# Kernel optimization log

Hardware: AMD Instinct MI355X
Metric: run time of the kernel (lower is better)

## Reference

```python
import jax, jax.numpy as jnp
import numpy as np

K = 3
STRIDE = 1
PAD = 1


def _conv(x, w, b):
    # NCHW conv, OIHW weight, stride/pad fixed
    y = jax.lax.conv_general_dilated(
        x, w, (STRIDE, STRIDE), [(PAD, PAD), (PAD, PAD)],
        dimension_numbers=("NCHW", "OIHW", "NCHW"))
    if b is not None:
        y = y + b[None, :, None, None]
    return y


def _deform_conv2d(x, offset, mask, weight):
    """torchvision.ops.deform_conv2d (modulated, groups=1, dilation=1, no bias)."""
    B, C, H, W = x.shape
    O = weight.shape[0]
    KK = K * K
    Ho, Wo = offset.shape[2], offset.shape[3]
    off = offset.reshape(B, KK, 2, Ho, Wo)
    off_y, off_x = off[:, :, 0], off[:, :, 1]
    ky = (jnp.arange(KK) // K).astype(x.dtype)  # kernel row offset
    kx = (jnp.arange(KK) % K).astype(x.dtype)   # kernel col offset
    base_y = (jnp.arange(Ho) * STRIDE - PAD).astype(x.dtype)
    base_x = (jnp.arange(Wo) * STRIDE - PAD).astype(x.dtype)
    # sampling positions [B, KK, Ho, Wo]
    py = base_y[None, None, :, None] + ky[None, :, None, None] + off_y
    px = base_x[None, None, None, :] + kx[None, :, None, None] + off_x

    y0 = jnp.floor(py)
    x0 = jnp.floor(px)
    wy = py - y0  # fractional parts
    wx = px - x0

    x_flat = x.reshape(B, C, H * W)

    def gather(yy, xx):
        valid = (yy >= 0) & (yy < H) & (xx >= 0) & (xx < W)
        yc = jnp.clip(yy, 0, H - 1).astype(jnp.int32)
        xc = jnp.clip(xx, 0, W - 1).astype(jnp.int32)
        idx = (yc * W + xc).reshape(B, -1)  # [B, KK*Ho*Wo]
        v = jax.vmap(lambda a, i: a[:, i])(x_flat, idx)  # [B, C, KK*Ho*Wo]
        v = v.reshape(B, C, KK, Ho, Wo)
        return v * valid.astype(x.dtype).reshape(B, 1, KK, Ho, Wo)

    samp = (gather(y0, x0) * ((1 - wy) * (1 - wx))[:, None]
            + gather(y0, x0 + 1) * ((1 - wy) * wx)[:, None]
            + gather(y0 + 1, x0) * (wy * (1 - wx))[:, None]
            + gather(y0 + 1, x0 + 1) * (wy * wx)[:, None])
    samp = samp * mask[:, None]  # modulation [B, C, KK, Ho, Wo]
    return jnp.einsum('bckhw,ock->bohw', samp, weight.reshape(O, C, KK))


def setup_inputs() -> dict:
    key = jax.random.key(0)
    ks = jax.random.split(key, 6)
    B, Cin, H, W, Cout = 4, 128, 128, 128, 256
    KK = K * K
    x = jax.random.normal(ks[0], (B, Cin, H, W), dtype=jnp.float32)
    # offset conv: trained weights are small (init at 0) -> scale down
    offset_w = 0.01 * jax.random.normal(ks[1], (2 * KK, Cin, K, K), dtype=jnp.float32)
    offset_b = 0.1 * jax.random.normal(ks[2], (2 * KK,), dtype=jnp.float32)
    mod_w = 0.1 * jax.random.normal(ks[3], (KK, Cin, K, K), dtype=jnp.float32)
    mod_b = 0.1 * jax.random.normal(ks[4], (KK,), dtype=jnp.float32)
    fan_in = Cin * KK
    weight = jax.random.normal(ks[5], (Cout, Cin, K, K), dtype=jnp.float32) / np.sqrt(fan_in)
    return {"x": x, "offset_w": offset_w, "offset_b": offset_b,
            "mod_w": mod_w, "mod_b": mod_b, "weight": weight}


def reference(x, offset_w, offset_b, mod_w, mod_b, weight):
    offset = _conv(x, offset_w, offset_b)
    modulator = 2.0 * jax.nn.sigmoid(_conv(x, mod_w, mod_b))
    return _deform_conv2d(x, offset, modulator, weight)
```

## Files before the change

### kernel.cpp

```cpp
#include <hip/hip_runtime.h>
#include <hip/hip_bf16.h>
#include <math.h>

#define CIN 128
#define HH 128
#define WW 128
#define HWX (HH*WW)
#define COUT 256
#define NB 4

typedef __attribute__((ext_vector_type(8))) short short8;
typedef __attribute__((ext_vector_type(4))) float f32x4;
typedef __attribute__((ext_vector_type(8))) unsigned short ushort8;

__device__ __forceinline__ unsigned short f2bf(float f) {
    union { float f; unsigned int u; } c; c.f = f;
    unsigned int u = c.u + 0x7FFF + ((c.u >> 16) & 1);
    return (unsigned short)(u >> 16);
}
__device__ __forceinline__ float bf2f(unsigned short u) {
    union { unsigned int u; float f; } c; c.u = ((unsigned int)u) << 16;
    return c.f;
}

__global__ __launch_bounds__(256) void wimg_kernel(
    const float* __restrict__ wgt, unsigned short* __restrict__ wAi)
{
    int i = blockIdx.x * 256 + threadIdx.x;
    int j  = i & 7;
    int l  = (i >> 3) & 63;
    int mt = (i >> 9) & 15;
    int cc = (i >> 13) & 3;
    int kk = i >> 15;
    int o = mt * 16 + (l & 15);
    int c = cc * 32 + (l >> 4) * 8 + j;
    wAi[i] = f2bf(wgt[(o * CIN + c) * 9 + kk]);
}

__global__ __launch_bounds__(256) void wcimg_kernel(
    const float* __restrict__ offw, const float* __restrict__ modw,
    unsigned short* __restrict__ wCi)
{
    int i = blockIdx.x * 256 + threadIdx.x;
    if (i >= 36864) return;
    int j   = i & 7;
    int l   = (i >> 3) & 63;
    int mt  = (i >> 9) & 1;
    int q36 = i >> 10;
    int o = mt * 16 + (l & 15);
    int c = ((q36 & 3) << 5) + ((l >> 4) << 3) + j;
    int t = q36 >> 2;
    float v = 0.f;
    if (o < 18)      v = offw[(o * CIN + c) * 9 + t];
    else if (o < 27) v = modw[((o - 18) * CIN + c) * 9 + t];
    wCi[i] = f2bf(v);
}

__global__ __launch_bounds__(256) void xt_kernel(
    const float* __restrict__ x, float* __restrict__ xT)
{
    __shared__ float ls[32][132];
    const int tid = threadIdx.x;
    const int bz = blockIdx.x;
    const int cg = bz & 3;
    const int y  = (bz >> 2) & 127;
    const int b  = bz >> 9;
    {
        int c  = tid >> 3;
        int x0 = (tid & 7) << 4;
        const float* src = x + (((size_t)(b * CIN + (cg << 5) + c)) << 14) + (y << 7) + x0;
#pragma unroll
        for (int k = 0; k < 4; ++k)
            *(f32x4*)&ls[c][x0 + 4 * k] = *(const f32x4*)(src + 4 * k);
    }
    __syncthreads();
    {
        int xc = tid >> 1;
        int h  = tid & 1;
        float v[16];
#pragma unroll
        for (int j = 0; j < 16; ++j) v[j] = ls[h * 16 + j][xc];
        float* dst = xT + ((((size_t)((b << 7) + y) << 7) + xc) << 7) + (cg << 5) + (h << 4);
#pragma unroll
        for (int k = 0; k < 4; ++k) {
            f32x4 t = { v[4 * k], v[4 * k + 1], v[4 * k + 2], v[4 * k + 3] };
            *(f32x4*)(dst + 4 * k) = t;
        }
    }
}

__global__ __launch_bounds__(256) void convtab_kernel(
    const float* __restrict__ xT, const unsigned short* __restrict__ wCi,
    const float* __restrict__ offb, const float* __restrict__ modb,
    unsigned int* __restrict__ pk_out, float4* __restrict__ w4_out)
{
    __shared__ float outs[4][32][33];
    const int tid = threadIdx.x;
    const int wave = tid >> 6;
    const int l = tid & 63;
    const int bid = blockIdx.x;
    const int b = bid >> 7;
    const int y = bid & 127;
    const int x0 = wave << 5;
    const float* xb = xT + ((size_t)b << 21);

    f32x4 acc[2][2];
#pragma unroll
    for (int i = 0; i < 2; ++i)
#pragma unroll
        for (int j = 0; j < 2; ++j) acc[i][j] = (f32x4){0.f, 0.f, 0.f, 0.f};

    const int lp = l & 15;
    const int q8 = (l >> 4) << 3;

#pragma unroll 1
    for (int q36 = 0; q36 < 36; ++q36) {
        const int t  = q36 >> 2;
        const int c0 = (q36 & 3) << 5;
        const int ty = t / 3, tx = t - 3 * ty;
        const int yp = y + ty - 1;
        if (yp < 0 || yp >= HH) continue;

        const unsigned short* ap = wCi + (q36 << 10) + (l << 3);
        short8 af0 = *(const short8*)(ap);
        short8 af1 = *(const short8*)(ap + 512);

        short8 bf[2];
#pragma unroll
        for (int nt = 0; nt < 2; ++nt) {
            int xp = x0 + nt * 16 + lp + tx - 1;
            bool xin = (xp >= 0) && (xp < WW);
            const float* src = xb +
                ((((yp << 7) + (xin ? xp : 0)) << 7) + c0 + q8);
            f32x4 z = {0.f, 0.f, 0.f, 0.f};
            f32x4 lo = xin ? *(const f32x4*)src : z;
            f32x4 hi = xin ? *(const f32x4*)(src + 4) : z;
            union { unsigned int u[4]; short8 s8; } cv;
            asm("v_cvt_pk_bf16_f32 %0, %1, %2" : "=v"(cv.u[0]) : "v"(lo[0]), "v"(lo[1]));
            asm("v_cvt_pk_bf16_f32 %0, %1, %2" : "=v"(cv.u[1]) : "v"(lo[2]), "v"(lo[3]));
            asm("v_cvt_pk_bf16_f32 %0, %1, %2" : "=v"(cv.u[2]) : "v"(hi[0]), "v"(hi[1]));
            asm("v_cvt_pk_bf16_f32 %0, %1, %2" : "=v"(cv.u[3]) : "v"(hi[2]), "v"(hi[3]));
            bf[nt] = cv.s8;
        }
        acc[0][0] = __builtin_amdgcn_mfma_f32_16x16x32_bf16(af0, bf[0], acc[0][0], 0, 0, 0);
        acc[1][0] = __builtin_amdgcn_mfma_f32_16x16x32_bf16(af1, bf[0], acc[1][0], 0, 0, 0);
        acc[0][1] = __builtin_amdgcn_mfma_f32_16x16x32_bf16(af0, bf[1], acc[0][1], 0, 0, 0);
        acc[1][1] = __builtin_amdgcn_mfma_f32_16x16x32_bf16(af1, bf[1], acc[1][1], 0, 0, 0);
    }

    float (*po)[33] = outs[wave];
#pragma unroll
    for (int mt = 0; mt < 2; ++mt)
#pragma unroll
        for (int nt = 0; nt < 2; ++nt)
#pragma unroll
            for (int r = 0; r < 4; ++r)
                po[nt * 16 + lp][mt * 16 + (l >> 4) * 4 + r] = acc[mt][nt][r];

    const int pxe = l & 31;
    const int xw = x0 + pxe;
    const float* pe = &outs[wave][pxe][0];
#pragma unroll 1
    for (int kk = (l >> 5); kk < 9; kk += 2) {
        float oy = pe[2 * kk]     + offb[2 * kk];
        float ox = pe[2 * kk + 1] + offb[2 * kk + 1];
        float mt_ = pe[18 + kk]   + modb[kk];

        float m = 2.f / (1.f + expf(-mt_));
        float py = (float)(y - 1 + kk / 3) + oy;
        float px = (float)(xw - 1 + kk % 3) + ox;
        float y0f = floorf(py), x0f = floorf(px);
        float wy = py - y0f, wx = px - x0f;
        int y0 = (int)y0f, x0i = (int)x0f;
        int y1 = y0 + 1, x1 = x0i + 1;
        float vy0 = (y0 >= 0 && y0 < HH) ? 1.f : 0.f;
        float vy1 = (y1 >= 0 && y1 < HH) ? 1.f : 0.f;
        float vx0 = (x0i >= 0 && x0i < WW) ? 1.f : 0.f;
        float vx1 = (x1 >= 0 && x1 < WW) ? 1.f : 0.f;
        float a  = m * (1.f - wy) * vy0;
        float bb = m * wy * vy1;
        float u  = (1.f - wx) * vx0;
        float vv = wx * vx1;
        int y0c = min(max(y0, 0), HH - 1), y1c = min(max(y1, 0), HH - 1);
        int x0c = min(max(x0i, 0), WW - 1), x1c = min(max(x1, 0), WW - 1);
        int cb = min(max(x0i, 0), WW - 2);
        float wl = ((x0c == cb) ? u : 0.f) + ((x1c == cb) ? vv : 0.f);
        float wr = ((x0c == cb + 1) ? u : 0.f) + ((x1c == cb + 1) ? vv : 0.f);
        unsigned int pkv = (unsigned)y0c | ((unsigned)y1c << 7) |
                           ((unsigned)cb << 14);
        int gid = ((b * 9 + kk) << 14) + (y << 7) + xw;
        pk_out[gid] = pkv;
        w4_out[gid] = make_float4(a * wl, a * wr, bb * wl, bb * wr);
    }
}

__global__ __launch_bounds__(256) void gather_kernel(
    const float* __restrict__ xT, const unsigned int* __restrict__ pk,
    const float4* __restrict__ w4, unsigned short* __restrict__ samp,
    int b0, int nb2)
{
    __shared__ unsigned char glds[4096];
    const int tid = threadIdx.x;
    const int wave = tid >> 6;
    const int l = tid & 63;
    unsigned char* wb = glds + (wave << 10);

    const int F = blockIdx.x;
    const int band = F % nb2;
    const int s = F / nb2;
    const int lb = band >> 1;
    const int b = b0 + lb;
    const int yh = band & 1;
    const int unit = s * 4 + wave;
    const int h = unit & 1;
    const int gb = unit >> 1;
    const int row = yh * 64 + (gb >> 3);
    const int gx16 = gb & 7;
    const int g = (lb << 10) + (row << 3) + gx16;
    const float* xb = xT + ((size_t)b << 21);
    unsigned short* sg0 = samp + (((size_t)g * 36) << 9);
    const float colf = (l >= 32) ? 1.f : 0.f;

    int gi = ((b * 9) << 14) + (row << 7) + (gx16 << 4) + (h << 3) + (l & 7);
    unsigned int tpk = pk[gi];
    float4 tw = w4[gi];

#pragma unroll 1
    for (int kk = 0; kk < 9; ++kk) {
        int gin = gi + ((kk < 8) ? 16384 : 0);
        unsigned int tpkn = pk[gin];
        float4 twn = w4[gin];

#pragma unroll
        for (int st = 0; st < 2; ++st) {
            f32x4 r0[4], r1[4];
            float cw0[4], cw1[4];
#pragma unroll
            for (int p = 0; p < 4; ++p) {
                const int idx = st * 4 + p;
                unsigned int pv = __shfl(tpk, idx);
                float wx_ = __shfl(tw.x, idx);
                float wy_ = __shfl(tw.y, idx);
                float wz_ = __shfl(tw.z, idx);
                float ww_ = __shfl(tw.w, idx);
                cw0[p] = fmaf(wy_ - wx_, colf, wx_);
                cw1[p] = fmaf(ww_ - wz_, colf, wz_);
                const int y0c = pv & 127;
                const int y1c = (pv >> 7) & 127;
                const int cb  = pv >> 14;
                const float* base0 = xb + ((((y0c << 7) + cb) << 7) + (l << 2));
                const float* base1 = xb + ((((y1c << 7) + cb) << 7) + (l << 2));
                r0[p] = *(const f32x4*)base0;
                r1[p] = *(const f32x4*)base1;
            }
#pragma unroll
            for (int p = 0; p < 4; ++p) {
                float res[4];
#pragma unroll
                for (int j = 0; j < 4; ++j) {
                    float t = r0[p][j] * cw0[p] + r1[p][j] * cw1[p];
                    res[j] = t + __shfl_xor(t, 32);
                }
                unsigned int d0 = (unsigned int)f2bf(res[0]) |
                                  ((unsigned int)f2bf(res[1]) << 16);
                unsigned int d1 = (unsigned int)f2bf(res[2]) |
                                  ((unsigned int)f2bf(res[3]) << 16);
                uint2 dd; dd.x = d0; dd.y = d1;
                *(uint2*)(wb + (p << 8) + ((l & 31) << 3)) = dd;
            }
            ushort8 chunk = *(ushort8*)(wb + ((l >> 4) << 8) + ((l & 15) << 4));
            const int px = (h << 3) + (st << 2) + (l >> 4);
            const int cc = (l & 15) >> 2;
            const int q  = l & 3;
            *(ushort8*)&sg0[((((kk << 2) + cc) << 6) + (q << 4) + px) << 3] =
                chunk;
        }
        tpk = tpkn; tw = twn;
        gi += 16384;
    }
}

__global__ __launch_bounds__(256) void dgemm_kernel(
    const unsigned short* __restrict__ wAi,
    const unsigned short* __restrict__ samp,
    float* __restrict__ out, int b0)
{
    const int tid = threadIdx.x;
    const int wave = tid >> 6;
    const int l = tid & 63;
    const int bx = blockIdx.x;
    const int lb = bx >> 8;
    const int b = b0 + lb;
    const int seg = bx & 255;
    const int pix0 = seg << 6;
    const unsigned short* sb =
        samp + (((size_t)((lb << 10) + (seg << 2)) * 36) << 9) + (l << 3);
    const int NTS = 36 << 9;

    f32x4 acc[4][4];
#pragma unroll
    for (int i = 0; i < 4; ++i)
#pragma unroll
        for (int j = 0; j < 4; ++j) acc[i][j] = (f32x4){0.f, 0.f, 0.f, 0.f};

    short8 bf[4], bfn[4];
#pragma unroll
    for (int nt = 0; nt < 4; ++nt)
        bf[nt] = *(const short8*)(sb + nt * NTS);

#pragma unroll 1
    for (int c36 = 0; c36 < 36; ++c36) {
        const unsigned short* ap = wAi + (c36 << 13) + (wave << 11) + (l << 3);
        short8 af[4];
#pragma unroll
        for (int mt = 0; mt < 4; ++mt)
            af[mt] = *(const short8*)(ap + (mt << 9));

        int cn = (c36 < 35) ? c36 + 1 : 35;
#pragma unroll
        for (int nt = 0; nt < 4; ++nt)
            bfn[nt] = *(const short8*)(sb + nt * NTS + (cn << 9));

#pragma unroll
        for (int mt = 0; mt < 4; ++mt)
#pragma unroll
            for (int nt = 0; nt < 4; ++nt)
                acc[mt][nt] = __builtin_amdgcn_mfma_f32_16x16x32_bf16(
                    af[mt], bf[nt], acc[mt][nt], 0, 0, 0);

#pragma unroll
        for (int nt = 0; nt < 4; ++nt) bf[nt] = bfn[nt];
    }

    const int crow = (l >> 4) * 4;
    const int pxl = pix0 + (l & 15);
#pragma unroll
    for (int mt = 0; mt < 4; ++mt) {
#pragma unroll
        for (int nt = 0; nt < 4; ++nt) {
#pragma unroll
            for (int r = 0; r < 4; ++r) {
                int o = wave * 64 + mt * 16 + crow + r;
                out[(((size_t)(b * COUT + o)) << 14) + pxl + nt * 16] =
                    acc[mt][nt][r];
            }
        }
    }
}

extern "C" void kernel_launch(void* const* d_in, const int* in_sizes, int n_in,
                              void* d_out, int out_size, void* d_ws, size_t ws_size,
                              hipStream_t stream)
{
    const float* x    = (const float*)d_in[0];
    const float* offw = (const float*)d_in[1];
    const float* offb = (const float*)d_in[2];
    const float* modw = (const float*)d_in[3];
    const float* modb = (const float*)d_in[4];
    const float* wgt  = (const float*)d_in[5];
    float* out = (float*)d_out;

    char* wsb = (char*)d_ws;
    unsigned int*   pkp = (unsigned int*)wsb;
    float4*         w4p = (float4*)(wsb + 2359296);
    unsigned short* wAi = (unsigned short*)(wsb + 11796480);
    unsigned short* wCi = (unsigned short*)(wsb + 12386304);
    float*          xTp = (float*)(wsb + 12460032);
    const size_t persistX = 12460032 + 33554432;
    unsigned short* samp = (unsigned short*)(wsb + persistX);
    const size_t SAMP1 = 37748736;

    int nb = 4;
    if (ws_size < persistX + 4 * SAMP1) nb = 2;
    if (ws_size < persistX + 2 * SAMP1) nb = 1;

    wimg_kernel<<<dim3(COUT * CIN * 9 / 256), 256, 0, stream>>>(wgt, wAi);
    wcimg_kernel<<<dim3(144), 256, 0, stream>>>(offw, modw, wCi);
    xt_kernel<<<dim3(NB * 128 * 4), 256, 0, stream>>>(x, xTp);
    convtab_kernel<<<dim3(NB * HH), 256, 0, stream>>>(
        xTp, wCi, offb, modb, pkp, w4p);

    for (int b0 = 0; b0 < NB; b0 += nb) {
        gather_kernel<<<dim3(nb * 512), 256, 0, stream>>>(
            xTp, pkp, w4p, samp, b0, nb * 2);
        dgemm_kernel<<<dim3(nb * 256), 256, 0, stream>>>(wAi, samp, out, b0);
    }
}
```

Measured before the change: 281.6 us.

## Fuse bilinear gather with bf16 MFMA GEMM through double-buffered LDS

Replaces the separate gather kernel, which wrote bf16 sampled columns to a global workspace, and the GEMM kernel that read them back, with one fused kernel. Each block gathers the sampled tile for one kernel tap into a double-buffered LDS tile while running MFMAs on the previous tap. Blocks are remapped with a swizzle. Float-to-bf16 conversion now uses the hardware packed convert instruction instead of software rounding. This removes the large global round trip and the per-batch launches, in exchange for more LDS use, barriers, and gather latency that sits inside the GEMM loop.

```diff
diff --git a/kernel.cpp b/kernel.cpp
--- a/kernel.cpp
+++ b/kernel.cpp
@@ -17,10 +17,6 @@
     union { float f; unsigned int u; } c; c.f = f;
     unsigned int u = c.u + 0x7FFF + ((c.u >> 16) & 1);
     return (unsigned short)(u >> 16);
-}
-__device__ __forceinline__ float bf2f(unsigned short u) {
-    union { unsigned int u; float f; } c; c.u = ((unsigned int)u) << 16;
-    return c.f;
 }
 
 __global__ __launch_bounds__(256) void wimg_kernel(
@@ -194,64 +190,60 @@
     }
 }
 
-__global__ __launch_bounds__(256) void gather_kernel(
-    const float* __restrict__ xT, const unsigned int* __restrict__ pk,
-    const float4* __restrict__ w4, unsigned short* __restrict__ samp,
-    int b0, int nb2)
-{
-    __shared__ unsigned char glds[4096];
+__global__ __launch_bounds__(256, 2) void fused_kernel(
+    const float* __restrict__ xT, const unsigned short* __restrict__ wAi,
+    const unsigned int* __restrict__ pk, const float4* __restrict__ w4,
+    float* __restrict__ out)
+{
+    __shared__ unsigned short Blds[2][4][4][512];
+    __shared__ unsigned char bounce[4][1024];
+
     const int tid = threadIdx.x;
-    const int wave = tid >> 6;
+    const int wv = tid >> 6;
     const int l = tid & 63;
-    unsigned char* wb = glds + (wave << 10);
-
-    const int F = blockIdx.x;
-    const int band = F % nb2;
-    const int s = F / nb2;
-    const int lb = band >> 1;
-    const int b = b0 + lb;
-    const int yh = band & 1;
-    const int unit = s * 4 + wave;
-    const int h = unit & 1;
-    const int gb = unit >> 1;
-    const int row = yh * 64 + (gb >> 3);
-    const int gx16 = gb & 7;
-    const int g = (lb << 10) + (row << 3) + gx16;
-    const float* xb = xT + ((size_t)b << 21);
-    unsigned short* sg0 = samp + (((size_t)g * 36) << 9);
+    const int bx = blockIdx.x;
+    const int S = ((bx & 7) << 7) + (bx >> 3);
+    const int lb = S >> 8;
+    const int seg = S & 255;
+    const int y = seg >> 1;
+    const int x0 = (seg & 1) << 6;
+    const float* xb = xT + ((size_t)lb << 21);
+    unsigned char* wb = bounce[wv];
     const float colf = (l >= 32) ? 1.f : 0.f;
 
-    int gi = ((b * 9) << 14) + (row << 7) + (gx16 << 4) + (h << 3) + (l & 7);
+    int gi = ((lb * 9) << 14) + (y << 7) + x0 + (wv << 4) + (l & 15);
     unsigned int tpk = pk[gi];
     float4 tw = w4[gi];
 
-#pragma unroll 1
-    for (int kk = 0; kk < 9; ++kk) {
+    f32x4 acc[4][4];
+#pragma unroll
+    for (int i = 0; i < 4; ++i)
+#pragma unroll
+        for (int j = 0; j < 4; ++j) acc[i][j] = (f32x4){0.f, 0.f, 0.f, 0.f};
+
+    auto produce = [&](int kk, int buf) {
         int gin = gi + ((kk < 8) ? 16384 : 0);
         unsigned int tpkn = pk[gin];
         float4 twn = w4[gin];
-
-#pragma unroll
-        for (int st = 0; st < 2; ++st) {
+#pragma unroll
+        for (int st = 0; st < 4; ++st) {
             f32x4 r0[4], r1[4];
             float cw0[4], cw1[4];
 #pragma unroll
             for (int p = 0; p < 4; ++p) {
                 const int idx = st * 4 + p;
                 unsigned int pv = __shfl(tpk, idx);
-                float wx_ = __shfl(tw.x, idx);
-                float wy_ = __shfl(tw.y, idx);
-                float wz_ = __shfl(tw.z, idx);
-                float ww_ = __shfl(tw.w, idx);
-                cw0[p] = fmaf(wy_ - wx_, colf, wx_);
-                cw1[p] = fmaf(ww_ - wz_, colf, wz_);
+                float wxx = __shfl(tw.x, idx);
+                float wyy = __shfl(tw.y, idx);
+                float wzz = __shfl(tw.z, idx);
+                float www = __shfl(tw.w, idx);
+                cw0[p] = fmaf(wyy - wxx, colf, wxx);
+                cw1[p] = fmaf(www - wzz, colf, wzz);
                 const int y0c = pv & 127;
                 const int y1c = (pv >> 7) & 127;
                 const int cb  = pv >> 14;
-                const float* base0 = xb + ((((y0c << 7) + cb) << 7) + (l << 2));
-                const float* base1 = xb + ((((y1c << 7) + cb) << 7) + (l << 2));
-                r0[p] = *(const f32x4*)base0;
-                r1[p] = *(const f32x4*)base1;
+                r0[p] = *(const f32x4*)(xb + ((((y0c << 7) + cb) << 7) + (l << 2)));
+                r1[p] = *(const f32x4*)(xb + ((((y1c << 7) + cb) << 7) + (l << 2)));
             }
 #pragma unroll
             for (int p = 0; p < 4; ++p) {
@@ -261,87 +253,60 @@
                     float t = r0[p][j] * cw0[p] + r1[p][j] * cw1[p];
                     res[j] = t + __shfl_xor(t, 32);
                 }
-                unsigned int d0 = (unsigned int)f2bf(res[0]) |
-                                  ((unsigned int)f2bf(res[1]) << 16);
-                unsigned int d1 = (unsigned int)f2bf(res[2]) |
-                                  ((unsigned int)f2bf(res[3]) << 16);
+                unsigned int d0, d1;
+                asm("v_cvt_pk_bf16_f32 %0, %1, %2" : "=v"(d0) : "v"(res[0]), "v"(res[1]));
+                asm("v_cvt_pk_bf16_f32 %0, %1, %2" : "=v"(d1) : "v"(res[2]), "v"(res[3]));
                 uint2 dd; dd.x = d0; dd.y = d1;
                 *(uint2*)(wb + (p << 8) + ((l & 31) << 3)) = dd;
             }
             ushort8 chunk = *(ushort8*)(wb + ((l >> 4) << 8) + ((l & 15) << 4));
-            const int px = (h << 3) + (st << 2) + (l >> 4);
+            const int pxg = (st << 2) + (l >> 4);
             const int cc = (l & 15) >> 2;
             const int q  = l & 3;
-            *(ushort8*)&sg0[((((kk << 2) + cc) << 6) + (q << 4) + px) << 3] =
-                chunk;
-        }
-        tpk = tpkn; tw = twn;
-        gi += 16384;
-    }
-}
-
-__global__ __launch_bounds__(256) void dgemm_kernel(
-    const unsigned short* __restrict__ wAi,
-    const unsigned short* __restrict__ samp,
-    float* __restrict__ out, int b0)
-{
-    const int tid = threadIdx.x;
-    const int wave = tid >> 6;
-    const int l = tid & 63;
-    const int bx = blockIdx.x;
-    const int lb = bx >> 8;
-    const int b = b0 + lb;
-    const int seg = bx & 255;
-    const int pix0 = seg << 6;
-    const unsigned short* sb =
-        samp + (((size_t)((lb << 10) + (seg << 2)) * 36) << 9) + (l << 3);
-    const int NTS = 36 << 9;
-
-    f32x4 acc[4][4];
-#pragma unroll
-    for (int i = 0; i < 4; ++i)
-#pragma unroll
-        for (int j = 0; j < 4; ++j) acc[i][j] = (f32x4){0.f, 0.f, 0.f, 0.f};
-
-    short8 bf[4], bfn[4];
-#pragma unroll
-    for (int nt = 0; nt < 4; ++nt)
-        bf[nt] = *(const short8*)(sb + nt * NTS);
+            *(ushort8*)&Blds[buf][cc][wv][((q << 4) + pxg) << 3] = chunk;
+        }
+        tpk = tpkn; tw = twn; gi += 16384;
+    };
+
+    produce(0, 0);
+    __syncthreads();
 
 #pragma unroll 1
-    for (int c36 = 0; c36 < 36; ++c36) {
-        const unsigned short* ap = wAi + (c36 << 13) + (wave << 11) + (l << 3);
-        short8 af[4];
-#pragma unroll
-        for (int mt = 0; mt < 4; ++mt)
-            af[mt] = *(const short8*)(ap + (mt << 9));
-
-        int cn = (c36 < 35) ? c36 + 1 : 35;
-#pragma unroll
-        for (int nt = 0; nt < 4; ++nt)
-            bfn[nt] = *(const short8*)(sb + nt * NTS + (cn << 9));
-
-#pragma unroll
-        for (int mt = 0; mt < 4; ++mt)
+    for (int kk = 0; kk < 9; ++kk) {
+        const int buf = kk & 1;
+        if (kk < 8) produce(kk + 1, buf ^ 1);
+#pragma unroll
+        for (int cc = 0; cc < 4; ++cc) {
+            const unsigned short* ap =
+                wAi + (((kk << 2) + cc) << 13) + (wv << 11) + (l << 3);
+            short8 af[4];
+#pragma unroll
+            for (int mt = 0; mt < 4; ++mt)
+                af[mt] = *(const short8*)(ap + (mt << 9));
+            short8 bfr[4];
 #pragma unroll
             for (int nt = 0; nt < 4; ++nt)
-                acc[mt][nt] = __builtin_amdgcn_mfma_f32_16x16x32_bf16(
-                    af[mt], bf[nt], acc[mt][nt], 0, 0, 0);
-
-#pragma unroll
-        for (int nt = 0; nt < 4; ++nt) bf[nt] = bfn[nt];
+                bfr[nt] = *(const short8*)&Blds[buf][cc][nt][l << 3];
+#pragma unroll
+            for (int mt = 0; mt < 4; ++mt)
+#pragma unroll
+                for (int nt = 0; nt < 4; ++nt)
+                    acc[mt][nt] = __builtin_amdgcn_mfma_f32_16x16x32_bf16(
+                        af[mt], bfr[nt], acc[mt][nt], 0, 0, 0);
+        }
+        __syncthreads();
     }
 
     const int crow = (l >> 4) * 4;
-    const int pxl = pix0 + (l & 15);
+    const int pxl = (seg << 6) + (l & 15);
 #pragma unroll
     for (int mt = 0; mt < 4; ++mt) {
 #pragma unroll
         for (int nt = 0; nt < 4; ++nt) {
 #pragma unroll
             for (int r = 0; r < 4; ++r) {
-                int o = wave * 64 + mt * 16 + crow + r;
-                out[(((size_t)(b * COUT + o)) << 14) + pxl + nt * 16] =
+                int o = wv * 64 + mt * 16 + crow + r;
+                out[(((size_t)(lb * COUT + o)) << 14) + pxl + nt * 16] =
                     acc[mt][nt][r];
             }
         }
@@ -366,23 +331,12 @@
     unsigned short* wAi = (unsigned short*)(wsb + 11796480);
     unsigned short* wCi = (unsigned short*)(wsb + 12386304);
     float*          xTp = (float*)(wsb + 12460032);
-    const size_t persistX = 12460032 + 33554432;
-    unsigned short* samp = (unsigned short*)(wsb + persistX);
-    const size_t SAMP1 = 37748736;
-
-    int nb = 4;
-    if (ws_size < persistX + 4 * SAMP1) nb = 2;
-    if (ws_size < persistX + 2 * SAMP1) nb = 1;
 
     wimg_kernel<<<dim3(COUT * CIN * 9 / 256), 256, 0, stream>>>(wgt, wAi);
     wcimg_kernel<<<dim3(144), 256, 0, stream>>>(offw, modw, wCi);
     xt_kernel<<<dim3(NB * 128 * 4), 256, 0, stream>>>(x, xTp);
     convtab_kernel<<<dim3(NB * HH), 256, 0, stream>>>(
         xTp, wCi, offb, modb, pkp, w4p);
-
-    for (int b0 = 0; b0 < NB; b0 += nb) {
-        gather_kernel<<<dim3(nb * 512), 256, 0, stream>>>(
-            xTp, pkp, w4p, samp, b0, nb * 2);
-        dgemm_kernel<<<dim3(nb * 256), 256, 0, stream>>>(wAi, samp, out, b0);
-    }
-}
+    fused_kernel<<<dim3(NB * 256), 256, 0, stream>>>(
+        xTp, wAi, pkp, w4p, out);
+}
```

Result: faster. 258.6 us (-8.2%).
